# Kernel tuning notes

Measured on AMD Instinct MI355X. Metric: run time of the kernel, lower is better.

## Reference

```python
import jax, jax.numpy as jnp
import numpy as np

N_NODES = 100000
N_EDGES = 1600000
DIM_IN, DIM_HID, DIM_OUT = 64, 128, 40


def setup_inputs() -> dict:
    key = jax.random.key(0)
    ks = jax.random.split(key, 6)
    x = jax.random.normal(ks[0], (N_NODES, DIM_IN), dtype=jnp.float32)
    edge_index = jax.random.randint(ks[1], (2, N_EDGES), 0, N_NODES, dtype=jnp.int64)
    s_in = 1.0 / np.sqrt(DIM_IN)
    s_hid = 1.0 / np.sqrt(DIM_HID)
    W1l = jax.random.normal(ks[2], (DIM_HID, DIM_IN), dtype=jnp.float32) * s_in
    W1r = jax.random.normal(ks[3], (DIM_HID, DIM_IN), dtype=jnp.float32) * s_in
    b1 = jnp.zeros((DIM_HID,), dtype=jnp.float32)
    W2l = jax.random.normal(ks[4], (DIM_OUT, DIM_HID), dtype=jnp.float32) * s_hid
    W2r = jax.random.normal(ks[5], (DIM_OUT, DIM_HID), dtype=jnp.float32) * s_hid
    b2 = jnp.zeros((DIM_OUT,), dtype=jnp.float32)
    return {"x": x, "edge_index": edge_index, "W1l": W1l, "b1": b1,
            "W1r": W1r, "W2l": W2l, "b2": b2, "W2r": W2r}


def _sage_conv(h, src, dst, Wl, bl, Wr, n_nodes):
    # mean aggregation of source-node features into target nodes
    msg = h[src]                                      # [E, d]
    agg = jax.ops.segment_sum(msg, dst, num_segments=n_nodes)
    cnt = jax.ops.segment_sum(jnp.ones((src.shape[0],), h.dtype), dst,
                              num_segments=n_nodes)
    agg = agg / jnp.maximum(cnt, 1.0)[:, None]        # [N, d]
    # PyG SAGEConv: lin_l(agg) + bias + lin_r(x) (root weight, no bias)
    return agg @ Wl.T + bl + h @ Wr.T


def reference(x, edge_index, W1l, b1, W1r, W2l, b2, W2r):
    src, dst = edge_index[0], edge_index[1]
    n = x.shape[0]
    h = _sage_conv(x, src, dst, W1l, b1, W1r, n)
    h = jax.nn.relu(h)
    out = _sage_conv(h, src, dst, W2l, b2, W2r, n)
    return jax.nn.log_softmax(out, axis=-1)
```

## Files before the change

kernel.cpp:

```cpp
#include <hip/hip_runtime.h>
#include <math.h>

#define NN 100000
#define DI 64
#define DH 128
#define DO 40

#define NBUCK 512
#define NPB 196
#define CAP 3712
#define CAPP 4352
#define EPB 4096
#define TPB_S 512
#define KE (EPB / TPB_S)

typedef __attribute__((ext_vector_type(8))) short bf16x8;
typedef __attribute__((ext_vector_type(4))) float f32x4;
typedef __attribute__((ext_vector_type(2))) float f32x2;

__device__ __forceinline__ unsigned short bf16r(float a) {
    unsigned u = __float_as_uint(a);
    u = (u + 0x7FFF + ((u >> 16) & 1)) >> 16;
    return (unsigned short)u;
}
__device__ __forceinline__ unsigned bf16pair(float a, float b) {
    return (unsigned)bf16r(a) | ((unsigned)bf16r(b) << 16);
}
__device__ __forceinline__ float bflo(unsigned u) { return __uint_as_float(u << 16); }
__device__ __forceinline__ float bfhi(unsigned u) { return __uint_as_float(u & 0xFFFF0000u); }

__global__ __launch_bounds__(TPB_S) void setup_scatter_kernel(
        const float* __restrict__ x, const float* __restrict__ W1l,
        const float* __restrict__ W1r, const float* __restrict__ W2l,
        const float* __restrict__ W2r,
        unsigned* __restrict__ xb, unsigned short* __restrict__ WB1,
        unsigned short* __restrict__ WB2, unsigned* __restrict__ p2,
        const int* __restrict__ src, const int* __restrict__ dst,
        int* __restrict__ bcur, int* __restrict__ eb,
        int nbe, int E, int N) {
    __shared__ int h[NBUCK];
    int t = threadIdx.x;
    if ((int)blockIdx.x < nbe) {
        if (t < NBUCK) h[t] = 0;
        __syncthreads();
        int base = blockIdx.x * EPB;
        int end = base + EPB; if (end > E) end = E;
        int dloc[KE];
#pragma unroll
        for (int k = 0; k < KE; k++) {
            int i = base + t + k * TPB_S;
            dloc[k] = (i < end) ? dst[i] : -1;
        }
#pragma unroll
        for (int k = 0; k < KE; k++)
            if (dloc[k] >= 0) atomicAdd(&h[(unsigned)dloc[k] / NPB], 1);
        __syncthreads();
        if (t < NBUCK) {
            int v = h[t];
            h[t] = v ? (atomicAdd(&bcur[t], v) + t * CAP) : 0;
        }
        __syncthreads();
#pragma unroll
        for (int k = 0; k < KE; k++) {
            int d = dloc[k];
            if (d >= 0) {
                unsigned bk = (unsigned)d / NPB;
                int local = d - (int)bk * NPB;
                int pos = atomicAdd(&h[bk], 1);
                eb[pos] = (local << 17) | src[base + t + k * TPB_S];
            }
        }
    } else {
        int idx = (blockIdx.x - nbe) * TPB_S + t;
        if (idx < (N + 1) * 32) {
            if (idx < N * 32) {
                float2 f = ((const float2*)x)[idx];
                xb[idx] = bf16pair(f.x, f.y);
            } else {
                xb[idx] = 0;
            }
        }
        if (idx < 16384) {
            int j = idx & 7, lane = (idx >> 3) & 63, ks = (idx >> 9) & 3, nt = idx >> 11;
            int k = ks * 32 + (lane >> 4) * 8 + j;
            int n = nt * 16 + (lane & 15);
            float v = (k < DI) ? W1l[n * DI + k] : W1r[n * DI + (k - DI)];
            WB1[idx] = bf16r(v);
        }
        if (idx >= 16384 && idx < 16384 + 10240) {
            int idx2 = idx - 16384;
            int j = idx2 & 7, lane = (idx2 >> 3) & 63, ks = (idx2 >> 9) & 3, nt = idx2 >> 11;
            int k = ks * 32 + (lane >> 4) * 8 + j;
            int n = nt * 16 + (lane & 15);
            float v = (n < DO) ? W2l[n * DH + k] : W2r[(n - DO) * DH + k];
            WB2[idx2] = bf16r(v);
        }
        if (idx < 10) p2[(size_t)N * 10 + idx] = 0;
    }
}

__global__ __launch_bounds__(256) void bucket_fill_kernel(const int* __restrict__ eb,
                                                          const int* __restrict__ bend,
                                                          int* __restrict__ rowptr,
                                                          int* __restrict__ cntg,
                                                          float* __restrict__ inv,
                                                          int* __restrict__ col, int N) {
    __shared__ int scnt[256];
    __shared__ int scur[256];
    __shared__ int sbase[256];
    int b = blockIdx.x, t = threadIdx.x;
    int ebeg = b * CAP, eend = ebeg + bend[b];
    scnt[t] = 0;
    __syncthreads();
    for (int i = ebeg + t; i < eend; i += 256)
        atomicAdd(&scnt[eb[i] >> 17], 1);
    __syncthreads();
    int myc = scnt[t];
    int pc = (myc + 3) & ~3;
    scnt[t] = pc;
    __syncthreads();
    for (int off = 1; off < 256; off <<= 1) {
        int tmp = (t >= off) ? scnt[t - off] : 0;
        __syncthreads();
        scnt[t] += tmp;
        __syncthreads();
    }
    int excl = scnt[t] - pc;
    int base = b * CAPP + excl;
    int node = b * NPB + t;
    if (t < NPB && node < N) {
        rowptr[node] = base;
        cntg[node] = myc;
        inv[node] = 1.0f / (float)(myc > 0 ? myc : 1);
    }
    scur[t] = base;
    sbase[t] = base;
    __syncthreads();
    for (int i = ebeg + t; i < eend; i += 256) {
        int pk = eb[i];
        int pos = atomicAdd(&scur[pk >> 17], 1);
        col[pos] = pk & 0x1FFFF;
    }
    __syncthreads();
    if (t < NPB) {
        int bs = sbase[t];
        for (int i = myc; i < pc; i++) col[bs + i] = NN;
    }
}

__global__ __launch_bounds__(256) void agg_gemm12_kernel(
        const unsigned* __restrict__ xb, const int* __restrict__ rowptr,
        const int* __restrict__ cnt, const float* __restrict__ inv,
        const int* __restrict__ col,
        const unsigned short* __restrict__ WB1, const float* __restrict__ b1,
        const unsigned short* __restrict__ WB2, const float* __restrict__ b2,
        unsigned* __restrict__ p2, float* __restrict__ selfp, int N) {
    __shared__ unsigned short sh[64][136];
    __shared__ float st[64][41];
    int t = threadIdx.x;
    int g = t >> 3, chunk = t & 7;

#pragma unroll
    for (int it = 0; it < 2; ++it) {
        int lr = it * 32 + g;
        int n = blockIdx.x * 64 + lr;
        float a[8];
#pragma unroll
        for (int j = 0; j < 8; j++) a[j] = 0.f;
        float invn = 0.f;
        uint4 u = make_uint4(0, 0, 0, 0);
        if (n < N) {
            int beg = rowptr[n], deg = cnt[n];
            int degp = (deg + 3) & ~3;
            for (int i = 0; i < degp; i += 4) {
                int s0 = col[beg + i], s1 = col[beg + i + 1];
                int s2 = col[beg + i + 2], s3 = col[beg + i + 3];
                uint4 u0 = *(const uint4*)(xb + (size_t)s0 * 32 + chunk * 4);
                uint4 u1 = *(const uint4*)(xb + (size_t)s1 * 32 + chunk * 4);
                uint4 u2 = *(const uint4*)(xb + (size_t)s2 * 32 + chunk * 4);
                uint4 u3 = *(const uint4*)(xb + (size_t)s3 * 32 + chunk * 4);
                a[0] += bflo(u0.x) + bflo(u1.x) + bflo(u2.x) + bflo(u3.x);
                a[1] += bfhi(u0.x) + bfhi(u1.x) + bfhi(u2.x) + bfhi(u3.x);
                a[2] += bflo(u0.y) + bflo(u1.y) + bflo(u2.y) + bflo(u3.y);
                a[3] += bfhi(u0.y) + bfhi(u1.y) + bfhi(u2.y) + bfhi(u3.y);
                a[4] += bflo(u0.z) + bflo(u1.z) + bflo(u2.z) + bflo(u3.z);
                a[5] += bfhi(u0.z) + bfhi(u1.z) + bfhi(u2.z) + bfhi(u3.z);
                a[6] += bflo(u0.w) + bflo(u1.w) + bflo(u2.w) + bflo(u3.w);
                a[7] += bfhi(u0.w) + bfhi(u1.w) + bfhi(u2.w) + bfhi(u3.w);
            }
            invn = inv[n];
            u = *(const uint4*)(xb + (size_t)n * 32 + chunk * 4);
        }
        uint4 o;
        o.x = bf16pair(a[0] * invn, a[1] * invn);
        o.y = bf16pair(a[2] * invn, a[3] * invn);
        o.z = bf16pair(a[4] * invn, a[5] * invn);
        o.w = bf16pair(a[6] * invn, a[7] * invn);
        *(uint4*)&sh[lr][chunk * 8] = o;
        *(uint4*)&sh[lr][64 + chunk * 8] = u;
    }
    __syncthreads();

    int w = t >> 6, lane = t & 63;
    int quad = lane >> 4, m = lane & 15;
    int rbase = blockIdx.x * 64 + w * 16;
    int lw = w * 16;

    f32x4 acc[8];
#pragma unroll
    for (int nt = 0; nt < 8; nt++) acc[nt] = (f32x4)(0.f);
#pragma unroll
    for (int ks = 0; ks < 4; ks++) {
        bf16x8 a = *(const bf16x8*)(&sh[lw + m][ks * 32 + quad * 8]);
#pragma unroll
        for (int nt = 0; nt < 8; nt++) {
            bf16x8 b = *(const bf16x8*)(WB1 + ((size_t)(nt * 4 + ks) * 64 + lane) * 8);
            acc[nt] = __builtin_amdgcn_mfma_f32_16x16x32_bf16(a, b, acc[nt], 0, 0, 0);
        }
    }
    __syncthreads();
#pragma unroll
    for (int nt = 0; nt < 8; nt++) {
        int colj = nt * 16 + m;
        float bj = b1[colj];
#pragma unroll
        for (int r = 0; r < 4; r++) {
            sh[lw + quad * 4 + r][colj] = bf16r(fmaxf(acc[nt][r] + bj, 0.f));
        }
    }
    __syncthreads();

    f32x4 acc2[5];
#pragma unroll
    for (int nt = 0; nt < 5; nt++) acc2[nt] = (f32x4)(0.f);
#pragma unroll
    for (int ks = 0; ks < 4; ks++) {
        bf16x8 a = *(const bf16x8*)(&sh[lw + m][ks * 32 + quad * 8]);
#pragma unroll
        for (int nt = 0; nt < 5; nt++) {
            bf16x8 b = *(const bf16x8*)(WB2 + ((size_t)(nt * 4 + ks) * 64 + lane) * 8);
            acc2[nt] = __builtin_amdgcn_mfma_f32_16x16x32_bf16(a, b, acc2[nt], 0, 0, 0);
        }
    }
#pragma unroll
    for (int nt = 0; nt < 5; nt++) {
        int colj = nt * 16 + m;
#pragma unroll
        for (int r = 0; r < 4; r++) {
            int lrow = lw + quad * 4 + r;
            int row = rbase + quad * 4 + r;
            float v = acc2[nt][r];
            if (colj < 40) {
                st[lrow][colj] = v;
            } else if (row < N) {
                selfp[(size_t)row * 40 + (colj - 40)] = v + b2[colj - 40];
            }
        }
    }
    __syncthreads();
    for (int i = t; i < 64 * 10; i += 256) {
        int lr = i / 10, dw = i - lr * 10;
        int grow = blockIdx.x * 64 + lr;
        if (grow < N) {
            float v0 = st[lr][dw * 4 + 0], v1 = st[lr][dw * 4 + 1];
            float v2 = st[lr][dw * 4 + 2], v3 = st[lr][dw * 4 + 3];
            unsigned u = __builtin_amdgcn_cvt_pk_fp8_f32(v0, v1, 0u, false);
            u = __builtin_amdgcn_cvt_pk_fp8_f32(v2, v3, u, true);
            p2[(size_t)grow * 10 + dw] = u;
        }
    }
}

__global__ void agg2_softmax_kernel(const unsigned* __restrict__ p2,
                                    const float* __restrict__ selfp,
                                    const int* __restrict__ rowptr,
                                    const int* __restrict__ cnt,
                                    const float* __restrict__ inv,
                                    const int* __restrict__ col,
                                    float* __restrict__ out, int N) {
    int n = (blockIdx.x * 256 + threadIdx.x) >> 3;
    int chunk = threadIdx.x & 7;
    if (n >= N) return;
    int beg = rowptr[n], deg = cnt[n];
    int degp = (deg + 3) & ~3;
    bool vc = (chunk < 5);
    float a[8];
#pragma unroll
    for (int j = 0; j < 8; j++) a[j] = 0.f;
    for (int i = 0; i < degp; i += 4) {
        int s0 = col[beg + i], s1 = col[beg + i + 1];
        int s2 = col[beg + i + 2], s3 = col[beg + i + 3];
        if (vc) {
            uint2 u0 = *(const uint2*)(p2 + (size_t)s0 * 10 + chunk * 2);
            uint2 u1 = *(const uint2*)(p2 + (size_t)s1 * 10 + chunk * 2);
            uint2 u2 = *(const uint2*)(p2 + (size_t)s2 * 10 + chunk * 2);
            uint2 u3 = *(const uint2*)(p2 + (size_t)s3 * 10 + chunk * 2);
            f32x2 d;
            d = __builtin_amdgcn_cvt_pk_f32_fp8(u0.x, false); a[0] += d.x; a[1] += d.y;
            d = __builtin_amdgcn_cvt_pk_f32_fp8(u0.x, true);  a[2] += d.x; a[3] += d.y;
            d = __builtin_amdgcn_cvt_pk_f32_fp8(u0.y, false); a[4] += d.x; a[5] += d.y;
            d = __builtin_amdgcn_cvt_pk_f32_fp8(u0.y, true);  a[6] += d.x; a[7] += d.y;
            d = __builtin_amdgcn_cvt_pk_f32_fp8(u1.x, false); a[0] += d.x; a[1] += d.y;
            d = __builtin_amdgcn_cvt_pk_f32_fp8(u1.x, true);  a[2] += d.x; a[3] += d.y;
            d = __builtin_amdgcn_cvt_pk_f32_fp8(u1.y, false); a[4] += d.x; a[5] += d.y;
            d = __builtin_amdgcn_cvt_pk_f32_fp8(u1.y, true);  a[6] += d.x; a[7] += d.y;
            d = __builtin_amdgcn_cvt_pk_f32_fp8(u2.x, false); a[0] += d.x; a[1] += d.y;
            d = __builtin_amdgcn_cvt_pk_f32_fp8(u2.x, true);  a[2] += d.x; a[3] += d.y;
            d = __builtin_amdgcn_cvt_pk_f32_fp8(u2.y, false); a[4] += d.x; a[5] += d.y;
            d = __builtin_amdgcn_cvt_pk_f32_fp8(u2.y, true);  a[6] += d.x; a[7] += d.y;
            d = __builtin_amdgcn_cvt_pk_f32_fp8(u3.x, false); a[0] += d.x; a[1] += d.y;
            d = __builtin_amdgcn_cvt_pk_f32_fp8(u3.x, true);  a[2] += d.x; a[3] += d.y;
            d = __builtin_amdgcn_cvt_pk_f32_fp8(u3.y, false); a[4] += d.x; a[5] += d.y;
            d = __builtin_amdgcn_cvt_pk_f32_fp8(u3.y, true);  a[6] += d.x; a[7] += d.y;
        }
    }
    float invn = inv[n];
    float v[8];
    if (vc) {
        float4 s0 = *(const float4*)(selfp + (size_t)n * DO + chunk * 8);
        float4 s1 = *(const float4*)(selfp + (size_t)n * DO + chunk * 8 + 4);
        v[0] = a[0] * invn + s0.x; v[1] = a[1] * invn + s0.y;
        v[2] = a[2] * invn + s0.z; v[3] = a[3] * invn + s0.w;
        v[4] = a[4] * invn + s1.x; v[5] = a[5] * invn + s1.y;
        v[6] = a[6] * invn + s1.z; v[7] = a[7] * invn + s1.w;
    } else {
#pragma unroll
        for (int j = 0; j < 8; j++) v[j] = 0.f;
    }
    float mv = -INFINITY;
    if (vc) {
#pragma unroll
        for (int j = 0; j < 8; j++) mv = fmaxf(mv, v[j]);
    }
#pragma unroll
    for (int off = 1; off <= 4; off <<= 1) mv = fmaxf(mv, __shfl_xor(mv, off, 8));
    float es = 0.f;
    if (vc) {
#pragma unroll
        for (int j = 0; j < 8; j++) es += expf(v[j] - mv);
    }
#pragma unroll
    for (int off = 1; off <= 4; off <<= 1) es += __shfl_xor(es, off, 8);
    if (vc) {
        float ls = mv + logf(es);
        float4 o0, o1;
        o0.x = v[0] - ls; o0.y = v[1] - ls; o0.z = v[2] - ls; o0.w = v[3] - ls;
        o1.x = v[4] - ls; o1.y = v[5] - ls; o1.z = v[6] - ls; o1.w = v[7] - ls;
        *(float4*)(out + (size_t)n * DO + chunk * 8) = o0;
        *(float4*)(out + (size_t)n * DO + chunk * 8 + 4) = o1;
    }
}

extern "C" void kernel_launch(void* const* d_in, const int* in_sizes, int n_in,
                              void* d_out, int out_size, void* d_ws, size_t ws_size,
                              hipStream_t stream) {
    const float* x   = (const float*)d_in[0];
    const int*  ei   = (const int*)d_in[1];
    const float* W1l = (const float*)d_in[2];
    const float* b1  = (const float*)d_in[3];
    const float* W1r = (const float*)d_in[4];
    const float* W2l = (const float*)d_in[5];
    const float* b2  = (const float*)d_in[6];
    const float* W2r = (const float*)d_in[7];
    float* out = (float*)d_out;

    const int E = in_sizes[1] / 2;
    const int N = NN;
    const int* src = ei;
    const int* dst = ei + E;
    const int nbe = (E + EPB - 1) / EPB;
    const int nsetup = ((N + 1) * 32 + TPB_S - 1) / TPB_S;

    size_t off = 0;
    auto alloc = [&](size_t nf) { size_t o = off; off += (nf + 63) & ~(size_t)63; return o; };
    size_t o_bcur   = alloc(NBUCK);
    size_t o_eb     = alloc((size_t)NBUCK * CAP);
    size_t o_col    = alloc((size_t)NBUCK * CAPP);
    size_t o_rowptr = alloc(N);
    size_t o_cnt    = alloc(N);
    size_t o_inv    = alloc(N);
    size_t o_xb     = alloc((size_t)(N + 1) * 32);
    size_t o_p2     = alloc((size_t)(N + 1) * 10);
    size_t o_selfp  = alloc((size_t)N * DO);
    size_t o_wb1    = alloc(16384 / 2);
    size_t o_wb2    = alloc(10240 / 2);
    (void)ws_size;

    float* ws = (float*)d_ws;
    int* bcur   = (int*)(ws + o_bcur);
    int* eb     = (int*)(ws + o_eb);
    int* col    = (int*)(ws + o_col);
    int* rowptr = (int*)(ws + o_rowptr);
    int* cnt    = (int*)(ws + o_cnt);
    float* inv  = ws + o_inv;
    unsigned* xb = (unsigned*)(ws + o_xb);
    unsigned* p2 = (unsigned*)(ws + o_p2);
    float* selfp = ws + o_selfp;
    unsigned short* WB1 = (unsigned short*)(ws + o_wb1);
    unsigned short* WB2 = (unsigned short*)(ws + o_wb2);

    hipMemsetAsync(bcur, 0, NBUCK * sizeof(int), stream);

    setup_scatter_kernel<<<nbe + nsetup, TPB_S, 0, stream>>>(
        x, W1l, W1r, W2l, W2r, xb, WB1, WB2, p2, src, dst, bcur, eb, nbe, E, N);

    bucket_fill_kernel<<<NBUCK, 256, 0, stream>>>(eb, bcur, rowptr, cnt, inv, col, N);

    agg_gemm12_kernel<<<(N + 63) / 64, 256, 0, stream>>>(
        xb, rowptr, cnt, inv, col, WB1, b1, WB2, b2, p2, selfp, N);

    agg2_softmax_kernel<<<(N * 8 + 255) / 256, 256, 0, stream>>>(p2, selfp, rowptr, cnt, inv, col, out, N);
}
```

Baseline: 199.6 us.

## Make fused GEMM kernel wave-local and widen layer-2 gather to 8 edges

The fused aggregate+GEMM kernel now assigns each wave exactly the 16 rows it later multiplies. All block-wide __syncthreads become compiler memory fences, and the fp32 staging buffer is folded into the shared bf16 tile, which reduces LDS use and removes block barriers. Column lists are now padded to multiples of 8 with a larger per-bucket capacity, so the layer-2 gather loop can issue 8 independent fp8 row loads per iteration for more memory-level parallelism. The trade-offs are more padded sentinel gathers and a reliance on wave-synchronous LDS ordering without explicit barriers.

```diff
diff --git a/kernel.cpp b/kernel.cpp
--- a/kernel.cpp
+++ b/kernel.cpp
@@ -9,7 +9,7 @@
 #define NBUCK 512
 #define NPB 196
 #define CAP 3712
-#define CAPP 4352
+#define CAPP 5120
 #define EPB 4096
 #define TPB_S 512
 #define KE (EPB / TPB_S)
@@ -116,7 +116,7 @@
         atomicAdd(&scnt[eb[i] >> 17], 1);
     __syncthreads();
     int myc = scnt[t];
-    int pc = (myc + 3) & ~3;
+    int pc = (myc + 7) & ~7;
     scnt[t] = pc;
     __syncthreads();
     for (int off = 1; off < 256; off <<= 1) {
@@ -156,13 +156,16 @@
         const unsigned short* __restrict__ WB2, const float* __restrict__ b2,
         unsigned* __restrict__ p2, float* __restrict__ selfp, int N) {
     __shared__ unsigned short sh[64][136];
-    __shared__ float st[64][41];
     int t = threadIdx.x;
-    int g = t >> 3, chunk = t & 7;
+    int w = t >> 6, lane = t & 63;
+    int lw = w * 16;
+    int g8 = (t >> 3) & 7;
+    int chunk = t & 7;
+    int rbase = blockIdx.x * 64 + lw;
 
 #pragma unroll
     for (int it = 0; it < 2; ++it) {
-        int lr = it * 32 + g;
+        int lr = lw + g8 + it * 8;
         int n = blockIdx.x * 64 + lr;
         float a[8];
 #pragma unroll
@@ -199,13 +202,9 @@
         *(uint4*)&sh[lr][chunk * 8] = o;
         *(uint4*)&sh[lr][64 + chunk * 8] = u;
     }
-    __syncthreads();
-
-    int w = t >> 6, lane = t & 63;
+    asm volatile("" ::: "memory");
+
     int quad = lane >> 4, m = lane & 15;
-    int rbase = blockIdx.x * 64 + w * 16;
-    int lw = w * 16;
-
     f32x4 acc[8];
 #pragma unroll
     for (int nt = 0; nt < 8; nt++) acc[nt] = (f32x4)(0.f);
@@ -218,7 +217,7 @@
             acc[nt] = __builtin_amdgcn_mfma_f32_16x16x32_bf16(a, b, acc[nt], 0, 0, 0);
         }
     }
-    __syncthreads();
+    asm volatile("" ::: "memory");
 #pragma unroll
     for (int nt = 0; nt < 8; nt++) {
         int colj = nt * 16 + m;
@@ -228,7 +227,7 @@
             sh[lw + quad * 4 + r][colj] = bf16r(fmaxf(acc[nt][r] + bj, 0.f));
         }
     }
-    __syncthreads();
+    asm volatile("" ::: "memory");
 
     f32x4 acc2[5];
 #pragma unroll
@@ -242,28 +241,29 @@
             acc2[nt] = __builtin_amdgcn_mfma_f32_16x16x32_bf16(a, b, acc2[nt], 0, 0, 0);
         }
     }
+    asm volatile("" ::: "memory");
+    float* stw = (float*)&sh[lw][0];
 #pragma unroll
     for (int nt = 0; nt < 5; nt++) {
         int colj = nt * 16 + m;
 #pragma unroll
         for (int r = 0; r < 4; r++) {
-            int lrow = lw + quad * 4 + r;
             int row = rbase + quad * 4 + r;
             float v = acc2[nt][r];
             if (colj < 40) {
-                st[lrow][colj] = v;
+                stw[(quad * 4 + r) * 41 + colj] = v;
             } else if (row < N) {
                 selfp[(size_t)row * 40 + (colj - 40)] = v + b2[colj - 40];
             }
         }
     }
-    __syncthreads();
-    for (int i = t; i < 64 * 10; i += 256) {
+    asm volatile("" ::: "memory");
+    for (int i = lane; i < 160; i += 64) {
         int lr = i / 10, dw = i - lr * 10;
-        int grow = blockIdx.x * 64 + lr;
+        int grow = rbase + lr;
         if (grow < N) {
-            float v0 = st[lr][dw * 4 + 0], v1 = st[lr][dw * 4 + 1];
-            float v2 = st[lr][dw * 4 + 2], v3 = st[lr][dw * 4 + 3];
+            float v0 = stw[lr * 41 + dw * 4 + 0], v1 = stw[lr * 41 + dw * 4 + 1];
+            float v2 = stw[lr * 41 + dw * 4 + 2], v3 = stw[lr * 41 + dw * 4 + 3];
             unsigned u = __builtin_amdgcn_cvt_pk_fp8_f32(v0, v1, 0u, false);
             u = __builtin_amdgcn_cvt_pk_fp8_f32(v2, v3, u, true);
             p2[(size_t)grow * 10 + dw] = u;
@@ -282,36 +282,28 @@
     int chunk = threadIdx.x & 7;
     if (n >= N) return;
     int beg = rowptr[n], deg = cnt[n];
-    int degp = (deg + 3) & ~3;
+    int degp = (deg + 7) & ~7;
     bool vc = (chunk < 5);
     float a[8];
 #pragma unroll
     for (int j = 0; j < 8; j++) a[j] = 0.f;
-    for (int i = 0; i < degp; i += 4) {
-        int s0 = col[beg + i], s1 = col[beg + i + 1];
-        int s2 = col[beg + i + 2], s3 = col[beg + i + 3];
+    for (int i = 0; i < degp; i += 8) {
+        int ss[8];
+#pragma unroll
+        for (int k = 0; k < 8; k++) ss[k] = col[beg + i + k];
         if (vc) {
-            uint2 u0 = *(const uint2*)(p2 + (size_t)s0 * 10 + chunk * 2);
-            uint2 u1 = *(const uint2*)(p2 + (size_t)s1 * 10 + chunk * 2);
-            uint2 u2 = *(const uint2*)(p2 + (size_t)s2 * 10 + chunk * 2);
-            uint2 u3 = *(const uint2*)(p2 + (size_t)s3 * 10 + chunk * 2);
-            f32x2 d;
-            d = __builtin_amdgcn_cvt_pk_f32_fp8(u0.x, false); a[0] += d.x; a[1] += d.y;
-            d = __builtin_amdgcn_cvt_pk_f32_fp8(u0.x, true);  a[2] += d.x; a[3] += d.y;
-            d = __builtin_amdgcn_cvt_pk_f32_fp8(u0.y, false); a[4] += d.x; a[5] += d.y;
-            d = __builtin_amdgcn_cvt_pk_f32_fp8(u0.y, true);  a[6] += d.x; a[7] += d.y;
-            d = __builtin_amdgcn_cvt_pk_f32_fp8(u1.x, false); a[0] += d.x; a[1] += d.y;
-            d = __builtin_amdgcn_cvt_pk_f32_fp8(u1.x, true);  a[2] += d.x; a[3] += d.y;
-            d = __builtin_amdgcn_cvt_pk_f32_fp8(u1.y, false); a[4] += d.x; a[5] += d.y;
-            d = __builtin_amdgcn_cvt_pk_f32_fp8(u1.y, true);  a[6] += d.x; a[7] += d.y;
-            d = __builtin_amdgcn_cvt_pk_f32_fp8(u2.x, false); a[0] += d.x; a[1] += d.y;
-            d = __builtin_amdgcn_cvt_pk_f32_fp8(u2.x, true);  a[2] += d.x; a[3] += d.y;
-            d = __builtin_amdgcn_cvt_pk_f32_fp8(u2.y, false); a[4] += d.x; a[5] += d.y;
-            d = __builtin_amdgcn_cvt_pk_f32_fp8(u2.y, true);  a[6] += d.x; a[7] += d.y;
-            d = __builtin_amdgcn_cvt_pk_f32_fp8(u3.x, false); a[0] += d.x; a[1] += d.y;
-            d = __builtin_amdgcn_cvt_pk_f32_fp8(u3.x, true);  a[2] += d.x; a[3] += d.y;
-            d = __builtin_amdgcn_cvt_pk_f32_fp8(u3.y, false); a[4] += d.x; a[5] += d.y;
-            d = __builtin_amdgcn_cvt_pk_f32_fp8(u3.y, true);  a[6] += d.x; a[7] += d.y;
+            uint2 uu[8];
+#pragma unroll
+            for (int k = 0; k < 8; k++)
+                uu[k] = *(const uint2*)(p2 + (size_t)ss[k] * 10 + chunk * 2);
+#pragma unroll
+            for (int k = 0; k < 8; k++) {
+                f32x2 d;
+                d = __builtin_amdgcn_cvt_pk_f32_fp8(uu[k].x, false); a[0] += d.x; a[1] += d.y;
+                d = __builtin_amdgcn_cvt_pk_f32_fp8(uu[k].x, true);  a[2] += d.x; a[3] += d.y;
+                d = __builtin_amdgcn_cvt_pk_f32_fp8(uu[k].y, false); a[4] += d.x; a[5] += d.y;
+                d = __builtin_amdgcn_cvt_pk_f32_fp8(uu[k].y, true);  a[6] += d.x; a[7] += d.y;
+            }
         }
     }
     float invn = inv[n];
```

After: 196.6 us. About the same (-1.5%).
